# Optimization experiments

Measured on AMD Instinct MI355X. Metric: run time of the kernel, lower is better.

Reference implementation:

```python
import jax, jax.numpy as jnp
import numpy as np

N, NS, B = 4096, 256, 2
X, Y, Z = 128, 128, 16
R = 4                      # compress_ratio per spatial axis
C, NC, H = 128, 20, 8      # feat dim, num classes, heads
DH = C // H
EPS = 1e-5


def setup_inputs() -> dict:
    rng = np.random.default_rng(0)
    gx_n, gy_n, gz_n = X // R, Y // R, Z // R
    # pick NS//B unique super-voxel cells per batch element
    cells = np.stack([rng.choice(gx_n * gy_n * gz_n, NS // B, replace=False) for _ in range(B)])
    gx = cells // (gy_n * gz_n)
    rem = cells % (gy_n * gz_n)
    gy, gz = rem // gz_n, rem % gz_n
    bidx = np.repeat(np.arange(B), NS // B)
    sv = np.stack([bidx, gx.ravel(), gy.ravel(), gz.ravel()], axis=1)  # [NS,4]
    per = N // NS  # 16 voxels per super-voxel, distinct offsets in the 4x4x4 cell
    offs = np.argsort(rng.random((NS, R * R * R)), axis=1)[:, :per]
    dx, dy, dz = offs // (R * R), (offs // R) % R, offs % R
    vox = np.stack([
        np.repeat(sv[:, 0], per),
        (sv[:, 1, None] * R + dx).ravel(),
        (sv[:, 2, None] * R + dy).ravel(),
        (sv[:, 3, None] * R + dz).ravel()], axis=1).astype(np.int32)

    ks = jax.random.split(jax.random.key(0), 12)
    p = lambda k, shape, s=0.02: jax.random.normal(k, shape, jnp.float32) * s
    return dict(
        indices=jnp.asarray(vox),
        features=jax.random.normal(ks[0], (N, C), jnp.float32),
        cw1=p(ks[1], (C, C)), cb1=jnp.zeros(C), cg1=jnp.ones(C), cbe1=jnp.zeros(C),
        cw2=p(ks[2], (C, C)), cb2=jnp.zeros(C),
        pw1=p(ks[3], (3, 64)), pb1=jnp.zeros(64), pg1=jnp.ones(64), pbe1=jnp.zeros(64),
        pw2=p(ks[4], (64, 1)), pb2=jnp.zeros(1),
        wq=p(ks[5], (C, C)), bq=jnp.zeros(C),
        wk=p(ks[6], (C, C)), bk=jnp.zeros(C),
        wv=p(ks[7], (C, C)), bv=jnp.zeros(C),
        wo=p(ks[8], (C, C)), bo=jnp.zeros(C),
        ln_g=jnp.ones(C), ln_b=jnp.zeros(C),
        seg_w=p(ks[9], (3, 3, 3, C, NC)), seg_b=jnp.zeros(NC),
    )


def _bn(x, g, b):  # BatchNorm1d, training-mode batch statistics
    mu = x.mean(0)
    var = x.var(0)
    return (x - mu) * jax.lax.rsqrt(var + EPS) * g + b


def reference(indices, features, cw1, cb1, cg1, cbe1, cw2, cb2,
              pw1, pb1, pg1, pbe1, pw2, pb2,
              wq, bq, wk, bk, wv, bv, wo, bo, ln_g, ln_b, seg_w, seg_b):
    ratio = jnp.array([1, R, R, R], dtype=indices.dtype)
    comp = indices // ratio                                  # [N,4] super-voxel coord
    unq, inv = jnp.unique(comp, axis=0, size=NS, return_inverse=True)
    # scatter-add softmax(features) over super-voxels
    cf = jax.ops.segment_sum(jax.nn.softmax(features, axis=1), inv, num_segments=NS)
    h = jax.nn.relu(_bn(cf @ cw1 + cb1, cg1, cbe1)) @ cw2 + cb2      # [NS,C]
    # pairwise relative-position bias: tiny MLP over [N*NS,3]
    pos = (indices[:, None, 1:] - unq[None, :, 1:]).astype(jnp.float32).reshape(N * NS, 3)
    pbias = (jax.nn.relu(_bn(pos @ pw1 + pb1, pg1, pbe1)) @ pw2 + pb2).reshape(N, NS)
    # multi-head cross attention: voxels query super-voxels, bias added to scores
    q = (features @ wq + bq).reshape(N, H, DH)
    k = (h @ wk + bk).reshape(NS, H, DH)
    v = (h @ wv + bv).reshape(NS, H, DH)
    scores = jnp.einsum('nhd,shd->hns', q, k) / np.float32(np.sqrt(DH)) + pbias[None]
    attn = jax.nn.softmax(scores, axis=-1)                   # [H,N,NS]
    ctx = jnp.einsum('hns,shd->nhd', attn, v).reshape(N, C) @ wo + bo
    y = features + ctx                                       # residual + LayerNorm sublayer
    mu = y.mean(-1, keepdims=True)
    var = y.var(-1, keepdims=True)
    y = (y - mu) * jax.lax.rsqrt(var + EPS) * ln_g + ln_b
    # SubMConv3d(128->20, k=3, pad=1): dense scatter -> conv -> gather at active sites
    grid = jnp.zeros((B, X, Y, Z, C), jnp.float32).at[
        indices[:, 0], indices[:, 1], indices[:, 2], indices[:, 3]].set(y)
    out = jax.lax.conv_general_dilated(
        grid, seg_w, (1, 1, 1), 'SAME',
        dimension_numbers=('NDHWC', 'DHWIO', 'NDHWC')) + seg_b
    return out[indices[:, 0], indices[:, 1], indices[:, 2], indices[:, 3]]  # [N,NC]
```

## Files before the change

### kernel.cpp

```cpp
#include <hip/hip_runtime.h>

typedef unsigned short ushort_t;

#define NVOX 4096
#define NSV  256
#define XD   128
#define YD   128
#define ZD   16
#define CD   128
#define NCD  20
#define HD   8
#define DHD  16
#define MAPN 524288
#define EPSF 1e-5f

#define OF_FEAT 0
#define OF_CW1  524288
#define OF_CB1  540672
#define OF_CG1  540800
#define OF_CBE1 540928
#define OF_CW2  541056
#define OF_CB2  557440
#define OF_PW1  557568
#define OF_PB1  557760
#define OF_PG1  557824
#define OF_PBE1 557888
#define OF_PW2  557952
#define OF_PB2  558016
#define OF_WQ   558080
#define OF_BQ   574464
#define OF_WK   574592
#define OF_BK   590976
#define OF_WV   591104
#define OF_BV   607488
#define OF_WO   607616
#define OF_BO   624000
#define OF_LNG  624128
#define OF_LNB  624256
#define OF_SEGW 624384
#define OF_SEGB 693504
#define ARENA_N 693568
#define TOTCVT  624341

__device__ __forceinline__ float bf2f(const ushort_t* p){
  return __uint_as_float(((unsigned)(*p)) << 16);
}
__device__ __forceinline__ ushort_t f2bf(float f){
  unsigned u = __float_as_uint(f);
  u += 0x7fffu + ((u >> 16) & 1u);
  return (ushort_t)(u >> 16);
}
__device__ __forceinline__ unsigned pack2(float a, float b){
  return (unsigned)f2bf(a) | ((unsigned)f2bf(b) << 16);
}
__device__ __forceinline__ float unlo(unsigned u){ return __uint_as_float(u << 16); }
__device__ __forceinline__ float unhi(unsigned u){ return __uint_as_float(u & 0xffff0000u); }

struct SrcPtrs { const void* p[25]; };

__device__ const int g_cnt[25] = {524288,16384,128,128,128,16384,128,192,64,64,64,64,1,
                                  16384,128,16384,128,16384,128,16384,128,128,128,0,20};
__device__ const int g_off[25] = {OF_FEAT,OF_CW1,OF_CB1,OF_CG1,OF_CBE1,OF_CW2,OF_CB2,
                                  OF_PW1,OF_PB1,OF_PG1,OF_PBE1,OF_PW2,OF_PB2,
                                  OF_WQ,OF_BQ,OF_WK,OF_BK,OF_WV,OF_BV,OF_WO,OF_BO,
                                  OF_LNG,OF_LNB,OF_SEGW,OF_SEGB};

__device__ __forceinline__ float ldi(const void* p, int off, int fl){
  return fl ? bf2f((const ushort_t*)p + off) : ((const float*)p)[off];
}

struct SPREP {
  float frows[16][CD];
  float qpart[2][16][CD];
  float part[8][CD];
  float cfs[CD];
  float gpart[8][CD];
};
union __align__(16) UPREP { SPREP sv; int smom[18]; };

__global__ __launch_bounds__(512) void kprep(SrcPtrs sp, const int* idx, int* flag,
    float* arena, float* wt, int* map, float* afold_g, float* scfold_g,
    float* qb, float* t1T)
{
  __shared__ UPREP sm;
  __shared__ int sm_flag;
  int t = threadIdx.x, b = blockIdx.x;
  if (t < 64){
    const ushort_t* f16 = (const ushort_t*)sp.p[0];
    unsigned u = f16[2*t];
    int e = (u >> 7) & 0xFF;
    int sane = (u == 0 || (e >= 90 && e <= 150)) ? 1 : 0;
    unsigned long long bl = __ballot(sane);
    if (t == 0) sm_flag = (__popcll(bl) >= 48) ? 1 : 0;
  }
  __syncthreads();
  const int fl = sm_flag;

  if (b < 255){
    int gid = b*512 + t;
    const int GS = 255*512;
    if (gid == 0) *flag = fl;
    for (int k=gid; k<MAPN; k+=GS) map[k] = -1;
    for (int el=gid; el<TOTCVT; el+=GS){
      int s=0, rem=el;
      while (rem >= g_cnt[s]){ rem -= g_cnt[s]; ++s; }
      arena[g_off[s]+rem] = ldi(sp.p[s], rem, fl);
    }
    for (int k=gid; k<27*NCD*CD; k+=GS){
      int nb = k/(NCD*CD); int rem = k - nb*(NCD*CD); int o = rem/CD, i = rem - o*CD;
      wt[k] = ldi(sp.p[23], nb*(CD*NCD) + i*NCD + o, fl);
    }
  } else if (b < 511){
    int sv = b - 255;
    int rb = sv*16;
    if (fl){
      const uint2* fsrc = (const uint2*)((const ushort_t*)sp.p[0] + (size_t)rb*CD);
      uint2 u = fsrc[t];
      float* dst = &sm.sv.frows[t>>5][(t&31)*4];
      dst[0]=unlo(u.x); dst[1]=unhi(u.x); dst[2]=unlo(u.y); dst[3]=unhi(u.y);
    } else {
      const float4* fsrc = (const float4*)((const float*)sp.p[0] + (size_t)rb*CD);
      ((float4*)sm.sv.frows)[t] = fsrc[t];
    }
    __syncthreads();
    {
      int c8 = (t&15)*8, r = (t>>4)&15, kh = t>>8;
      int i0 = kh*64;
      float acc[8] = {0.f,0.f,0.f,0.f,0.f,0.f,0.f,0.f};
      if (fl){
        const ushort_t* wqp = (const ushort_t*)sp.p[13];
        #pragma unroll 4
        for (int i=i0; i<i0+64; ++i){
          uint4 w4 = *(const uint4*)(wqp + (size_t)i*CD + c8);
          float fr = sm.sv.frows[r][i];
          acc[0] += unlo(w4.x)*fr; acc[1] += unhi(w4.x)*fr;
          acc[2] += unlo(w4.y)*fr; acc[3] += unhi(w4.y)*fr;
          acc[4] += unlo(w4.z)*fr; acc[5] += unhi(w4.z)*fr;
          acc[6] += unlo(w4.w)*fr; acc[7] += unhi(w4.w)*fr;
        }
      } else {
        const float* wqp = (const float*)sp.p[13];
        #pragma unroll 4
        for (int i=i0; i<i0+64; ++i){
          float4 wa = *(const float4*)(wqp + (size_t)i*CD + c8);
          float4 wb = *(const float4*)(wqp + (size_t)i*CD + c8 + 4);
          float fr = sm.sv.frows[r][i];
          acc[0]+=wa.x*fr; acc[1]+=wa.y*fr; acc[2]+=wa.z*fr; acc[3]+=wa.w*fr;
          acc[4]+=wb.x*fr; acc[5]+=wb.y*fr; acc[6]+=wb.z*fr; acc[7]+=wb.w*fr;
        }
      }
      #pragma unroll
      for (int j=0;j<8;++j) sm.sv.qpart[kh][r][c8+j] = acc[j];
    }
    __syncthreads();
    for (int e = t; e < 16*CD; e += 512){
      int r = e>>7, c = e&127;
      qb[(size_t)(rb+r)*CD + c] = sm.sv.qpart[0][r][c] + sm.sv.qpart[1][r][c]
                                + ldi(sp.p[14], c, fl);
    }
    {
      int w = t>>6, l = t&63;
      float a0 = 0.f, a1 = 0.f;
      #pragma unroll
      for (int k=0;k<2;++k){
        int r = w*2 + k;
        float f0 = sm.sv.frows[r][l];
        float f1 = sm.sv.frows[r][l+64];
        float m = fmaxf(f0,f1);
        #pragma unroll
        for (int o=32;o;o>>=1) m = fmaxf(m, __shfl_xor(m,o,64));
        float e0 = __expf(f0-m), e1 = __expf(f1-m);
        float ssum = e0+e1;
        #pragma unroll
        for (int o=32;o;o>>=1) ssum += __shfl_xor(ssum,o,64);
        float inv = 1.f/ssum;
        a0 += e0*inv; a1 += e1*inv;
      }
      sm.sv.part[w][l] = a0; sm.sv.part[w][l+64] = a1;
    }
    __syncthreads();
    if (t < CD){
      float s = 0.f;
      #pragma unroll
      for (int w=0;w<8;++w) s += sm.sv.part[w][t];
      sm.sv.cfs[t] = s;
    }
    __syncthreads();
    {
      int c2 = (t&63)*2, kg = t>>6;
      int i0 = kg*16;
      float a0 = 0.f, a1 = 0.f;
      if (fl){
        const ushort_t* W = (const ushort_t*)sp.p[1];
        #pragma unroll 4
        for (int i=i0; i<i0+16; ++i){
          unsigned w = *(const unsigned*)(W + (size_t)i*CD + c2);
          float cfv = sm.sv.cfs[i];
          a0 += unlo(w)*cfv; a1 += unhi(w)*cfv;
        }
      } else {
        const float* W = (const float*)sp.p[1];
        #pragma unroll 4
        for (int i=i0; i<i0+16; ++i){
          float2 w = *(const float2*)(W + (size_t)i*CD + c2);
          float cfv = sm.sv.cfs[i];
          a0 += w.x*cfv; a1 += w.y*cfv;
        }
      }
      sm.sv.gpart[kg][c2] = a0; sm.sv.gpart[kg][c2+1] = a1;
    }
    __syncthreads();
    if (t < CD){
      float s = 0.f;
      #pragma unroll
      for (int kg=0;kg<8;++kg) s += sm.sv.gpart[kg][t];
      t1T[(size_t)t*NSV + sv] = s + ldi(sp.p[2], t, fl);
    }
  } else {
    if (t < 18) sm.smom[t] = 0;
    __syncthreads();
    int sacc[9] = {0,0,0,0,0,0,0,0,0};
    for (int v = t; v < NVOX; v += 512){
      int4 q = ((const int4*)idx)[v];
      sacc[0]+=q.y; sacc[1]+=q.z; sacc[2]+=q.w;
      sacc[3]+=q.y*q.y; sacc[4]+=q.z*q.z; sacc[5]+=q.w*q.w;
      sacc[6]+=q.y*q.z; sacc[7]+=q.y*q.w; sacc[8]+=q.z*q.w;
    }
    for (int i=0;i<9;++i) atomicAdd(&sm.smom[9+i], sacc[i]);
    if (t < 256){
      int4 q = ((const int4*)idx)[t*16];
      int gx=q.y>>2, gy=q.z>>2, gz=q.w>>2;
      atomicAdd(&sm.smom[0], gx); atomicAdd(&sm.smom[1], gy); atomicAdd(&sm.smom[2], gz);
      atomicAdd(&sm.smom[3], gx*gx); atomicAdd(&sm.smom[4], gy*gy); atomicAdd(&sm.smom[5], gz*gz);
      atomicAdd(&sm.smom[6], gx*gy); atomicAdd(&sm.smom[7], gx*gz); atomicAdd(&sm.smom[8], gy*gz);
    }
    __syncthreads();
    if (t < 64){
      int* smom = sm.smom;
      double U1[3]={(double)smom[0],(double)smom[1],(double)smom[2]};
      double S1[3]={(double)smom[9],(double)smom[10],(double)smom[11]};
      double Uxx[3][3], Sxx[3][3];
      Uxx[0][0]=smom[3]; Uxx[1][1]=smom[4]; Uxx[2][2]=smom[5];
      Uxx[0][1]=Uxx[1][0]=smom[6]; Uxx[0][2]=Uxx[2][0]=smom[7]; Uxx[1][2]=Uxx[2][1]=smom[8];
      Sxx[0][0]=smom[12]; Sxx[1][1]=smom[13]; Sxx[2][2]=smom[14];
      Sxx[0][1]=Sxx[1][0]=smom[15]; Sxx[0][2]=Sxx[2][0]=smom[16]; Sxx[1][2]=Sxx[2][1]=smom[17];
      double M1[3], M2[3][3];
      for (int a=0;a<3;++a) M1[a] = 256.0*S1[a] - 4096.0*U1[a];
      for (int a=0;a<3;++a)
        for (int b2=0;b2<3;++b2)
          M2[a][b2] = 256.0*Sxx[a][b2] - S1[a]*U1[b2] - S1[b2]*U1[a] + 4096.0*Uxx[a][b2];
      double wv_[3]={(double)ldi(sp.p[7],t,fl),(double)ldi(sp.p[7],64+t,fl),(double)ldi(sp.p[7],128+t,fl)};
      double bj=(double)ldi(sp.p[8],t,fl), gj=(double)ldi(sp.p[9],t,fl), bej=(double)ldi(sp.p[10],t,fl);
      double Mw=0.0, wMw=0.0;
      for (int a=0;a<3;++a){
        Mw += M1[a]*wv_[a];
        for (int b2=0;b2<3;++b2) wMw += wv_[a]*M2[a][b2]*wv_[b2];
      }
      const double NM = 1048576.0;
      double mean = Mw/NM + bj;
      double Ey2  = wMw/NM + 2.0*bj*Mw/NM + bj*bj;
      double var  = Ey2 - mean*mean;
      double scale = gj / sqrt(var + 1e-5);
      afold_g[t]      = (float)(wv_[0]*scale);
      afold_g[64+t]   = (float)(wv_[1]*scale);
      afold_g[128+t]  = (float)(wv_[2]*scale);
      scfold_g[t]     = (float)(bj*scale + bej - mean*scale);
    }
  }
}

__global__ __launch_bounds__(256) void k6_fused(const float* t1T, const float* A,
    const int* idx, int* map, float* kb, float* vb){
  __shared__ float row[CD];
  __shared__ float cpar[2][CD];
  __shared__ float hrow[CD];
  int t = threadIdx.x, s = blockIdx.x;
  if (t >= 128 && t < 144){
    int v = s*16 + (t-128);
    int4 q = ((const int4*)idx)[v];
    map[((q.x*XD + q.y)*YD + q.z)*ZD + q.w] = v;
  }
  if (t < CD){
    const float4* col = (const float4*)(t1T + (size_t)t*NSV);
    float sum=0.f, sq=0.f;
    #pragma unroll 8
    for (int i=0;i<NSV/4;++i){
      float4 v = col[i];
      sum += v.x+v.y+v.z+v.w;
      sq  += v.x*v.x+v.y*v.y+v.z*v.z+v.w*v.w;
    }
    float mean = sum*(1.f/256.f);
    float var  = sq*(1.f/256.f) - mean*mean;
    float scv = A[OF_CG1+t]*rsqrtf(var+EPSF);
    float shv = A[OF_CBE1+t] - mean*scv;
    row[t] = fmaxf(t1T[(size_t)t*NSV + s]*scv + shv, 0.f);
  }
  __syncthreads();
  int c = t&127, half = t>>7;
  {
    const float* W = A + OF_CW2;
    float acc = 0.f;
    #pragma unroll 8
    for (int i=half*64;i<half*64+64;++i) acc += row[i]*W[i*CD+c];
    cpar[half][c] = acc;
  }
  __syncthreads();
  if (t < CD) hrow[t] = cpar[0][t]+cpar[1][t]+A[OF_CB2+t];
  __syncthreads();
  {
    const float* W = half ? (A+OF_WV) : (A+OF_WK);
    float acc = half ? A[OF_BV+c] : A[OF_BK+c];
    #pragma unroll 8
    for (int i=0;i<CD;++i) acc += hrow[i]*W[i*CD+c];
    if (half) vb[(size_t)s*CD+c]=acc; else kb[(size_t)s*CD+c]=acc;
  }
}

__global__ __launch_bounds__(256) void k9_attn(
    const float* A, const int* idx, const float* afold_g, const float* scfold_g,
    const float* kb, const float* vb, const float* qb, float* yb)
{
  __shared__ __align__(16) float q4s[4][CD];
  __shared__ __align__(16) unsigned sc2[NSV][20];
  __shared__ __align__(16) float ctxT[CD*4];
  __shared__ float cpart[2][4][CD];
  __shared__ __align__(16) float e4T[64][4];
  __shared__ float saf[3][64];
  __shared__ float ssc[64];
  __shared__ float w2s[64];
  __shared__ float rinv[32];
  int t = threadIdx.x;
  int n0 = blockIdx.x*4;
  if (t < 128) ((float4*)q4s)[t] = ((const float4*)(qb + (size_t)n0*CD))[t];
  if (t < 64){
    saf[0][t] = afold_g[t]; saf[1][t] = afold_g[64+t]; saf[2][t] = afold_g[128+t];
    ssc[t] = scfold_g[t]; w2s[t] = A[OF_PW2+t];
  }
  __syncthreads();
  {
    int g = t>>6, j = t&63;
    float xv = (float)idx[4*(n0+g)+1];
    float yv = (float)idx[4*(n0+g)+2];
    float zv = (float)idx[4*(n0+g)+3];
    e4T[j][g] = saf[0][j]*xv + saf[1][j]*yv + saf[2][j]*zv;
  }
  __syncthreads();
  {
    int4 q0 = ((const int4*)idx)[t*16];
    float uxf = (float)(q0.y>>2), uyf = (float)(q0.z>>2), uzf = (float)(q0.w>>2);
    float pbv[4];
    float pb2v = A[OF_PB2];
    #pragma unroll
    for (int g=0;g<4;++g) pbv[g] = pb2v;
    #pragma unroll 2
    for (int j=0;j<64;++j){
      float dj = ssc[j] - (saf[0][j]*uxf + saf[1][j]*uyf + saf[2][j]*uzf);
      float wj = w2s[j];
      float4 ea = *(const float4*)&e4T[j][0];
      pbv[0] += fmaxf(ea.x+dj,0.f)*wj; pbv[1] += fmaxf(ea.y+dj,0.f)*wj;
      pbv[2] += fmaxf(ea.z+dj,0.f)*wj; pbv[3] += fmaxf(ea.w+dj,0.f)*wj;
    }
    const float4* krow = (const float4*)(kb + (size_t)t*CD);
    float4 kc0 = krow[0], kc1 = krow[1], kc2 = krow[2], kc3 = krow[3];
    for (int h=0;h<HD;++h){
      int hn = (h+1)&7;
      float4 kn0 = krow[hn*4+0], kn1 = krow[hn*4+1];
      float4 kn2 = krow[hn*4+2], kn3 = krow[hn*4+3];
      float p[4];
      #pragma unroll
      for (int g=0;g<4;++g){
        const float* qg = &q4s[g][h*DHD];
        float dot = qg[0]*kc0.x + qg[1]*kc0.y + qg[2]*kc0.z + qg[3]*kc0.w
                  + qg[4]*kc1.x + qg[5]*kc1.y + qg[6]*kc1.z + qg[7]*kc1.w
                  + qg[8]*kc2.x + qg[9]*kc2.y + qg[10]*kc2.z + qg[11]*kc2.w
                  + qg[12]*kc3.x + qg[13]*kc3.y + qg[14]*kc3.z + qg[15]*kc3.w;
        p[g] = __expf(dot*0.25f + pbv[g]);
      }
      sc2[t][h*2]   = pack2(p[0],p[1]);
      sc2[t][h*2+1] = pack2(p[2],p[3]);
      kc0 = kn0; kc1 = kn1; kc2 = kn2; kc3 = kn3;
    }
  }
  __syncthreads();
  {
    int g = t>>6, lane = t&63;
    int sel = g&1;
    for (int h=0;h<HD;++h){
      int col = h*2 + (g>>1);
      unsigned ua = sc2[lane][col];
      unsigned ub = sc2[lane+64][col];
      unsigned uc = sc2[lane+128][col];
      unsigned ud = sc2[lane+192][col];
      float s0 = sel ? (unhi(ua)+unhi(ub)+unhi(uc)+unhi(ud))
                     : (unlo(ua)+unlo(ub)+unlo(uc)+unlo(ud));
      #pragma unroll
      for (int o=32;o;o>>=1) s0 += __shfl_xor(s0,o,64);
      if (lane==0) rinv[g*8+h] = 1.f/s0;
    }
  }
  __syncthreads();
  {
    int half=t>>7, c=t&127, h=c>>4;
    const float* vcol = vb + c;
    float acc[4]={0.f,0.f,0.f,0.f};
    #pragma unroll 2
    for (int s0=half*128; s0<half*128+128; s0+=8){
      float v0=vcol[(s0+0)*CD], v1=vcol[(s0+1)*CD], v2=vcol[(s0+2)*CD], v3=vcol[(s0+3)*CD];
      float v4=vcol[(s0+4)*CD], v5=vcol[(s0+5)*CD], v6=vcol[(s0+6)*CD], v7=vcol[(s0+7)*CD];
      uint2 u0=*(const uint2*)&sc2[s0+0][h*2];
      uint2 u1=*(const uint2*)&sc2[s0+1][h*2];
      uint2 u2=*(const uint2*)&sc2[s0+2][h*2];
      uint2 u3=*(const uint2*)&sc2[s0+3][h*2];
      uint2 u4=*(const uint2*)&sc2[s0+4][h*2];
      uint2 u5=*(const uint2*)&sc2[s0+5][h*2];
      uint2 u6=*(const uint2*)&sc2[s0+6][h*2];
      uint2 u7=*(const uint2*)&sc2[s0+7][h*2];
      acc[0] += unlo(u0.x)*v0 + unlo(u1.x)*v1 + unlo(u2.x)*v2 + unlo(u3.x)*v3
              + unlo(u4.x)*v4 + unlo(u5.x)*v5 + unlo(u6.x)*v6 + unlo(u7.x)*v7;
      acc[1] += unhi(u0.x)*v0 + unhi(u1.x)*v1 + unhi(u2.x)*v2 + unhi(u3.x)*v3
              + unhi(u4.x)*v4 + unhi(u5.x)*v5 + unhi(u6.x)*v6 + unhi(u7.x)*v7;
      acc[2] += unlo(u0.y)*v0 + unlo(u1.y)*v1 + unlo(u2.y)*v2 + unlo(u3.y)*v3
              + unlo(u4.y)*v4 + unlo(u5.y)*v5 + unlo(u6.y)*v6 + unlo(u7.y)*v7;
      acc[3] += unhi(u0.y)*v0 + unhi(u1.y)*v1 + unhi(u2.y)*v2 + unhi(u3.y)*v3
              + unhi(u4.y)*v4 + unhi(u5.y)*v5 + unhi(u6.y)*v6 + unhi(u7.y)*v7;
    }
    #pragma unroll
    for (int g=0;g<4;++g) cpart[half][g][c]=acc[g];
  }
  __syncthreads();
  if (t < CD){
    int h = t>>4;
    #pragma unroll
    for (int g=0;g<4;++g)
      ctxT[t*4+g] = (cpart[0][g][t]+cpart[1][g][t])*rinv[g*8+h];
  }
  __syncthreads();
  {
    int half=t>>7, c=t&127;
    const float* wo = A + OF_WO;
    float acc[4]={0.f,0.f,0.f,0.f};
    #pragma unroll 4
    for (int i=half*64;i<half*64+64;++i){
      float wv = wo[i*CD+c];
      float4 r = *(const float4*)&ctxT[i*4];
      acc[0]+=r.x*wv; acc[1]+=r.y*wv; acc[2]+=r.z*wv; acc[3]+=r.w*wv;
    }
    #pragma unroll
    for (int g=0;g<4;++g) cpart[half][g][c]=acc[g];
  }
  __syncthreads();
  if (t < CD){
    float bov = A[OF_BO+t];
    #pragma unroll
    for (int g=0;g<4;++g)
      ctxT[t*4+g] = cpart[0][g][t]+cpart[1][g][t] + bov
                  + A[OF_FEAT + (size_t)(n0+g)*CD + t];
  }
  __syncthreads();
  {
    int g = t>>6, lane = t&63;
    float x0 = ctxT[lane*4+g], x1 = ctxT[(lane+64)*4+g];
    float s1 = x0+x1, s2 = x0*x0+x1*x1;
    #pragma unroll
    for (int o=32;o;o>>=1){ s1 += __shfl_xor(s1,o,64); s2 += __shfl_xor(s2,o,64); }
    float mean = s1*(1.f/128.f);
    float var  = s2*(1.f/128.f) - mean*mean;
    float rs = rsqrtf(var + EPSF);
    yb[(size_t)(n0+g)*CD + lane]    = (x0-mean)*rs*A[OF_LNG+lane]    + A[OF_LNB+lane];
    yb[(size_t)(n0+g)*CD + lane+64] = (x1-mean)*rs*A[OF_LNG+lane+64] + A[OF_LNB+lane+64];
  }
}

__global__ __launch_bounds__(256) void k10_conv(const int* idx, const int* map,
    const float* yb, const float* A, const float* wt, const int* flag, void* outv)
{
  __shared__ int sco4[8][4];
  __shared__ int jn[8][27];
  __shared__ float partial[4][8][NCD];
  int t = threadIdx.x;
  int p0 = blockIdx.x*8;
  if (t < 32) ((int*)sco4)[t] = idx[4*p0 + t];
  __syncthreads();
  if (t < 216){
    int v = t/27, nb = t - v*27;
    int kd = nb/9, kh = (nb/3)%3, kw = nb%3;
    int bb = sco4[v][0];
    int nx = sco4[v][1]+kd-1, ny = sco4[v][2]+kh-1, nz = sco4[v][3]+kw-1;
    int j = -1;
    if ((unsigned)nx < XD && (unsigned)ny < YD && (unsigned)nz < ZD)
      j = map[((bb*XD+nx)*YD+ny)*ZD+nz];
    jn[v][nb] = j;
  }
  __syncthreads();
  int w = t>>6, l = t&63;
  int og = l & 3, cg = l >> 2;
  int c0 = cg*8;
  float acc[8][5];
  #pragma unroll
  for (int v=0;v<8;++v)
    #pragma unroll
    for (int oo=0;oo<5;++oo) acc[v][oo]=0.f;
  for (int nb = w; nb < 27; nb += 4){
    const float* wbase = wt + (size_t)nb*NCD*CD + c0;
    float4 wreg[10];
    #pragma unroll
    for (int oo=0;oo<5;++oo){
      wreg[oo*2]   = *(const float4*)(wbase + (size_t)(og*5+oo)*CD);
      wreg[oo*2+1] = *(const float4*)(wbase + (size_t)(og*5+oo)*CD + 4);
    }
    #pragma unroll
    for (int v=0; v<8; ++v){
      int j = jn[v][nb];
      if (j < 0) continue;
      const float4* y4 = (const float4*)(yb + (size_t)j*CD + c0);
      float4 ya = y4[0], ybb = y4[1];
      #pragma unroll
      for (int oo=0;oo<5;++oo){
        float4 wa = wreg[oo*2], wb = wreg[oo*2+1];
        acc[v][oo] += ya.x*wa.x + ya.y*wa.y + ya.z*wa.z + ya.w*wa.w
                    + ybb.x*wb.x + ybb.y*wb.y + ybb.z*wb.z + ybb.w*wb.w;
      }
    }
  }
  #pragma unroll
  for (int v=0;v<8;++v)
    #pragma unroll
    for (int oo=0;oo<5;++oo){
      float s = acc[v][oo];
      s += __shfl_xor(s, 4, 64);
      s += __shfl_xor(s, 8, 64);
      s += __shfl_xor(s, 16, 64);
      s += __shfl_xor(s, 32, 64);
      if (cg == 0) partial[w][v][og*5+oo] = s;
    }
  __syncthreads();
  if (t < 160){
    int v = t/20, o = t - v*20;
    float s = partial[0][v][o]+partial[1][v][o]+partial[2][v][o]+partial[3][v][o]
            + A[OF_SEGB+o];
    if (*flag) ((ushort_t*)outv)[(size_t)(p0+v)*NCD + o] = f2bf(s);
    else       ((float*)outv)[(size_t)(p0+v)*NCD + o]   = s;
  }
}

extern "C" void kernel_launch(void* const* d_in, const int* in_sizes, int n_in,
                              void* d_out, int out_size, void* d_ws, size_t ws_size,
                              hipStream_t stream) {
  const int* idx = (const int*)d_in[0];

  char* w = (char*)d_ws;
  size_t off = 0;
  #define ALLOC(name, type, count) \
    type* name = (type*)(w + off); off += (((size_t)(count)*sizeof(type)) + 255) & ~(size_t)255;
  ALLOC(flag,   int,   64)
  ALLOC(arena,  float, ARENA_N)
  ALLOC(wt,     float, 27*NCD*CD)
  ALLOC(map,    int,   MAPN)
  ALLOC(afold,  float, 192)
  ALLOC(scfold, float, 64)
  ALLOC(t1T,    float, CD*NSV)
  ALLOC(kb,     float, NSV*CD)
  ALLOC(vbuf,   float, NSV*CD)
  ALLOC(qb,     float, NVOX*CD)
  ALLOC(yb,     float, NVOX*CD)
  #undef ALLOC
  (void)off; (void)ws_size; (void)n_in; (void)in_sizes; (void)out_size;

  SrcPtrs sp;
  for (int i=0;i<25;++i) sp.p[i] = d_in[i+1];

  kprep   <<<512, 512, 0, stream>>>(sp, idx, flag, arena, wt, map, afold, scfold, qb, t1T);
  k6_fused<<<NSV, 256, 0, stream>>>(t1T, arena, idx, map, kb, vbuf);
  k9_attn <<<NVOX/4, 256, 0, stream>>>(arena, idx, afold, scfold, kb, vbuf, qb, yb);
  k10_conv<<<NVOX/8, 256, 0, stream>>>(idx, map, yb, arena, wt, flag, d_out);
}
```

Measured before the change: 236.4 us.

## Store attention probabilities in fp32 and split K/V projection across blocks

The attention kernel now keeps the exponentiated scores in an fp32 shared buffer (padded rows of 36) instead of packing them as bf16 pairs. This removes the pack/unpack ALU work and lets the PV loop read float4 directly, at the cost of more shared memory per block and possibly lower occupancy. The K/V kernel launches twice as many blocks, one role each for K and V. Each block redundantly recomputes the BN+ReLU and the first linear layer, then splits the 128-length dot product across two thread halves with a shared-memory reduction.

```diff
diff --git a/kernel.cpp b/kernel.cpp
--- a/kernel.cpp
+++ b/kernel.cpp
@@ -49,9 +49,6 @@
   unsigned u = __float_as_uint(f);
   u += 0x7fffu + ((u >> 16) & 1u);
   return (ushort_t)(u >> 16);
-}
-__device__ __forceinline__ unsigned pack2(float a, float b){
-  return (unsigned)f2bf(a) | ((unsigned)f2bf(b) << 16);
 }
 __device__ __forceinline__ float unlo(unsigned u){ return __uint_as_float(u << 16); }
 __device__ __forceinline__ float unhi(unsigned u){ return __uint_as_float(u & 0xffff0000u); }
@@ -274,8 +271,9 @@
   __shared__ float row[CD];
   __shared__ float cpar[2][CD];
   __shared__ float hrow[CD];
-  int t = threadIdx.x, s = blockIdx.x;
-  if (t >= 128 && t < 144){
+  int t = threadIdx.x;
+  int role = blockIdx.x >> 8, s = blockIdx.x & 255;
+  if (role == 0 && t >= 128 && t < 144){
     int v = s*16 + (t-128);
     int4 q = ((const int4*)idx)[v];
     map[((q.x*XD + q.y)*YD + q.z)*ZD + q.w] = v;
@@ -308,11 +306,16 @@
   if (t < CD) hrow[t] = cpar[0][t]+cpar[1][t]+A[OF_CB2+t];
   __syncthreads();
   {
-    const float* W = half ? (A+OF_WV) : (A+OF_WK);
-    float acc = half ? A[OF_BV+c] : A[OF_BK+c];
+    const float* W = role ? (A+OF_WV) : (A+OF_WK);
+    float acc = 0.f;
     #pragma unroll 8
-    for (int i=0;i<CD;++i) acc += hrow[i]*W[i*CD+c];
-    if (half) vb[(size_t)s*CD+c]=acc; else kb[(size_t)s*CD+c]=acc;
+    for (int i=half*64;i<half*64+64;++i) acc += hrow[i]*W[i*CD+c];
+    cpar[half][c] = acc;
+  }
+  __syncthreads();
+  if (t < CD){
+    float v = cpar[0][t]+cpar[1][t] + (role ? A[OF_BV+t] : A[OF_BK+t]);
+    if (role) vb[(size_t)s*CD+t] = v; else kb[(size_t)s*CD+t] = v;
   }
 }
 
@@ -321,7 +324,7 @@
     const float* kb, const float* vb, const float* qb, float* yb)
 {
   __shared__ __align__(16) float q4s[4][CD];
-  __shared__ __align__(16) unsigned sc2[NSV][20];
+  __shared__ __align__(16) float scf[NSV][36];
   __shared__ __align__(16) float ctxT[CD*4];
   __shared__ float cpart[2][4][CD];
   __shared__ __align__(16) float e4T[64][4];
@@ -376,23 +379,16 @@
                   + qg[12]*kc3.x + qg[13]*kc3.y + qg[14]*kc3.z + qg[15]*kc3.w;
         p[g] = __expf(dot*0.25f + pbv[g]);
       }
-      sc2[t][h*2]   = pack2(p[0],p[1]);
-      sc2[t][h*2+1] = pack2(p[2],p[3]);
+      *(float4*)&scf[t][h*4] = make_float4(p[0],p[1],p[2],p[3]);
       kc0 = kn0; kc1 = kn1; kc2 = kn2; kc3 = kn3;
     }
   }
   __syncthreads();
   {
     int g = t>>6, lane = t&63;
-    int sel = g&1;
     for (int h=0;h<HD;++h){
-      int col = h*2 + (g>>1);
-      unsigned ua = sc2[lane][col];
-      unsigned ub = sc2[lane+64][col];
-      unsigned uc = sc2[lane+128][col];
-      unsigned ud = sc2[lane+192][col];
-      float s0 = sel ? (unhi(ua)+unhi(ub)+unhi(uc)+unhi(ud))
-                     : (unlo(ua)+unlo(ub)+unlo(uc)+unlo(ud));
+      int col = h*4 + g;
+      float s0 = scf[lane][col] + scf[lane+64][col] + scf[lane+128][col] + scf[lane+192][col];
       #pragma unroll
       for (int o=32;o;o>>=1) s0 += __shfl_xor(s0,o,64);
       if (lane==0) rinv[g*8+h] = 1.f/s0;
@@ -403,26 +399,17 @@
     int half=t>>7, c=t&127, h=c>>4;
     const float* vcol = vb + c;
     float acc[4]={0.f,0.f,0.f,0.f};
-    #pragma unroll 2
-    for (int s0=half*128; s0<half*128+128; s0+=8){
+    #pragma unroll 4
+    for (int s0=half*128; s0<half*128+128; s0+=4){
       float v0=vcol[(s0+0)*CD], v1=vcol[(s0+1)*CD], v2=vcol[(s0+2)*CD], v3=vcol[(s0+3)*CD];
-      float v4=vcol[(s0+4)*CD], v5=vcol[(s0+5)*CD], v6=vcol[(s0+6)*CD], v7=vcol[(s0+7)*CD];
-      uint2 u0=*(const uint2*)&sc2[s0+0][h*2];
-      uint2 u1=*(const uint2*)&sc2[s0+1][h*2];
-      uint2 u2=*(const uint2*)&sc2[s0+2][h*2];
-      uint2 u3=*(const uint2*)&sc2[s0+3][h*2];
-      uint2 u4=*(const uint2*)&sc2[s0+4][h*2];
-      uint2 u5=*(const uint2*)&sc2[s0+5][h*2];
-      uint2 u6=*(const uint2*)&sc2[s0+6][h*2];
-      uint2 u7=*(const uint2*)&sc2[s0+7][h*2];
-      acc[0] += unlo(u0.x)*v0 + unlo(u1.x)*v1 + unlo(u2.x)*v2 + unlo(u3.x)*v3
-              + unlo(u4.x)*v4 + unlo(u5.x)*v5 + unlo(u6.x)*v6 + unlo(u7.x)*v7;
-      acc[1] += unhi(u0.x)*v0 + unhi(u1.x)*v1 + unhi(u2.x)*v2 + unhi(u3.x)*v3
-              + unhi(u4.x)*v4 + unhi(u5.x)*v5 + unhi(u6.x)*v6 + unhi(u7.x)*v7;
-      acc[2] += unlo(u0.y)*v0 + unlo(u1.y)*v1 + unlo(u2.y)*v2 + unlo(u3.y)*v3
-              + unlo(u4.y)*v4 + unlo(u5.y)*v5 + unlo(u6.y)*v6 + unlo(u7.y)*v7;
-      acc[3] += unhi(u0.y)*v0 + unhi(u1.y)*v1 + unhi(u2.y)*v2 + unhi(u3.y)*v3
-              + unhi(u4.y)*v4 + unhi(u5.y)*v5 + unhi(u6.y)*v6 + unhi(u7.y)*v7;
+      float4 p0 = *(const float4*)&scf[s0+0][h*4];
+      float4 p1 = *(const float4*)&scf[s0+1][h*4];
+      float4 p2 = *(const float4*)&scf[s0+2][h*4];
+      float4 p3 = *(const float4*)&scf[s0+3][h*4];
+      acc[0] += p0.x*v0 + p1.x*v1 + p2.x*v2 + p3.x*v3;
+      acc[1] += p0.y*v0 + p1.y*v1 + p2.y*v2 + p3.y*v3;
+      acc[2] += p0.z*v0 + p1.z*v1 + p2.z*v2 + p3.z*v3;
+      acc[3] += p0.w*v0 + p1.w*v1 + p2.w*v2 + p3.w*v3;
     }
     #pragma unroll
     for (int g=0;g<4;++g) cpart[half][g][c]=acc[g];
@@ -570,7 +557,7 @@
   for (int i=0;i<25;++i) sp.p[i] = d_in[i+1];
 
   kprep   <<<512, 512, 0, stream>>>(sp, idx, flag, arena, wt, map, afold, scfold, qb, t1T);
-  k6_fused<<<NSV, 256, 0, stream>>>(t1T, arena, idx, map, kb, vbuf);
+  k6_fused<<<NSV*2, 256, 0, stream>>>(t1T, arena, idx, map, kb, vbuf);
   k9_attn <<<NVOX/4, 256, 0, stream>>>(arena, idx, afold, scfold, kb, vbuf, qb, yb);
   k10_conv<<<NVOX/8, 256, 0, stream>>>(idx, map, yb, arena, wt, flag, d_out);
 }
```

Result: slower. 242.8 us (+2.7%).
